# Kernel tuning notes

Measured on AMD Instinct MI355X. Metric: run time of the kernel, lower is better.

## Reference

```python
import jax, jax.numpy as jnp
import numpy as np

XI = 4.0  # init kwarg


def _gaussian_kernel(xi: float):
    radius = int(3 * xi)
    coords = jnp.arange(-radius, radius + 1, dtype=jnp.float32)
    g1 = jnp.exp(-coords ** 2 / (2 * xi * xi))
    g1 = g1 / g1.sum()
    # dense 3D outer-product kernel, shape (K, K, K)
    g3 = g1[:, None, None] * g1[None, :, None] * g1[None, None, :]
    K = g3.shape[0]
    # grouped depthwise weight: (out=3, in/groups=1, K, K, K)
    return jnp.broadcast_to(g3[None, None], (3, 1, K, K, K))


def setup_inputs() -> dict:
    key = jax.random.key(0)
    x = jax.random.normal(key, (1, 3, 160, 160, 160), dtype=jnp.float32)
    kernel = _gaussian_kernel(XI)
    return {"x": x, "kernel": kernel}


def reference(x, kernel):
    # grouped Conv3d, groups=3 (depthwise), 'same' padding of radius each side
    r = (kernel.shape[-1] - 1) // 2
    return jax.lax.conv_general_dilated(
        x, kernel,
        window_strides=(1, 1, 1),
        padding=[(r, r), (r, r), (r, r)],
        dimension_numbers=("NCDHW", "OIDHW", "NCDHW"),
        feature_group_count=3,
    )
```

## Files before the change

kernel.cpp:

```cpp
#include <hip/hip_runtime.h>
#include <hip/hip_fp16.h>


#define NV 160
constexpr int KS    = 25;
constexpr int RAD   = 12;
constexpr int PLANE = NV * NV;
constexpr int VOL   = NV * NV * NV;
constexpr int TOT   = 3 * VOL;
constexpr int ROWS  = NV + 2 * RAD;

constexpr int PITCH = 17;
constexpr int OPT   = 10;
constexpr int WIN   = OPT + KS - 1;

constexpr int QP    = 9;
constexpr int OPT4  = 5;
constexpr int WIN4  = OPT4 + KS - 1;

__device__ __forceinline__ void pk(float2& a, float2 g, float2 v) {
    asm("v_pk_fma_f32 %0, %1, %2, %0" : "+v"(a) : "v"(g), "v"(v));
}

__device__ __forceinline__ void load_g(const float* __restrict__ k3, float* g) {
    float c   = k3[12 * 625 + 312];
    float g12 = cbrtf(c);
    float inv = 1.0f / (g12 * g12);
#pragma unroll
    for (int t = 0; t < KS; ++t) g[t] = k3[t * 625 + 312] * inv;
}

__global__ __launch_bounds__(256) void conv_w(const float* __restrict__ in,
                                              __half* __restrict__ out,
                                              const float* __restrict__ k3) {
    __shared__ float2 T[ROWS][PITCH];
    float gs[KS];
    load_g(k3, gs);
    float2 g2[KS];
#pragma unroll
    for (int t = 0; t < KS; ++t) g2[t] = make_float2(gs[t], gs[t]);

    int tid = threadIdx.x;
    int b   = blockIdx.x;
    int ht  = b % 5;
    int cd  = b / 5;
    int h0  = ht * 32;
    const float* base = in + (size_t)cd * PLANE;

    int wl = tid & 31, hq = tid >> 5;
#pragma unroll
    for (int hh = 0; hh < 2; ++hh) {
        int hp = hq + hh * 8;
        const float* r0 = base + (h0 + 2 * hp) * NV;
#pragma unroll
        for (int ib = 0; ib < ROWS; ib += 32) {
            int i = ib + wl;
            if (i < ROWS) {
                int wv = i - RAD;
                float a = 0.f, bb = 0.f;
                if (wv >= 0 && wv < NV) { a = r0[wv]; bb = r0[NV + wv]; }
                T[i][hp] = make_float2(a, bb);
            }
        }
    }
    __syncthreads();

    int p  = tid & 15;
    int ct = tid >> 4;
    int wb = ct * OPT;
    float2 acc[OPT];
#pragma unroll
    for (int j = 0; j < OPT; ++j) acc[j] = make_float2(0.f, 0.f);
#pragma unroll
    for (int it = 0; it < WIN; ++it) {
        float2 v = T[wb + it][p];
#pragma unroll
        for (int j = 0; j < OPT; ++j) {
            int t = it - j;
            if (t >= 0 && t < KS) pk(acc[j], g2[t], v);
        }
    }
    __half* obA = out + (size_t)cd * PLANE + (h0 + 2 * p) * NV + wb;
#pragma unroll
    for (int jj = 0; jj < OPT / 2; ++jj) {
        *(__half2*)(obA + 2 * jj) =
            __float22half2_rn(make_float2(acc[2*jj].x, acc[2*jj+1].x));
        *(__half2*)(obA + NV + 2 * jj) =
            __float22half2_rn(make_float2(acc[2*jj].y, acc[2*jj+1].y));
    }
}

__global__ __launch_bounds__(256) void conv_h(const __half* __restrict__ in,
                                              __half* __restrict__ out,
                                              const float* __restrict__ k3) {
    __shared__ float4 T4[ROWS][QP];
    float gs[KS];
    load_g(k3, gs);
    float2 g2[KS];
#pragma unroll
    for (int t = 0; t < KS; ++t) g2[t] = make_float2(gs[t], gs[t]);

    int tid = threadIdx.x;
    int b   = blockIdx.x;
    int wt  = b % 5;
    int cd  = b / 5;
    int w0  = wt * 32;
    const __half* base = in + (size_t)cd * PLANE + w0;

    int q = tid & 7, r = tid >> 3;
#pragma unroll
    for (int ib = 0; ib < ROWS; ib += 32) {
        int i = ib + r;
        if (i < ROWS) {
            int h = i - RAD;
            float4 v = make_float4(0.f, 0.f, 0.f, 0.f);
            if (h >= 0 && h < NV) {
                const __half2* p2 = (const __half2*)(base + h * NV + 4 * q);
                float2 lo = __half22float2(p2[0]);
                float2 hi = __half22float2(p2[1]);
                v = make_float4(lo.x, lo.y, hi.x, hi.y);
            }
            T4[i][q] = v;
        }
    }
    __syncthreads();

    int wq = tid & 7, ct = tid >> 3;
    int hb = ct * OPT4;
    float2 alo[OPT4], ahi[OPT4];
#pragma unroll
    for (int j = 0; j < OPT4; ++j) { alo[j] = make_float2(0.f, 0.f); ahi[j] = alo[j]; }
#pragma unroll
    for (int it = 0; it < WIN4; ++it) {
        float4 v = T4[hb + it][wq];
        float2 vlo = make_float2(v.x, v.y);
        float2 vhi = make_float2(v.z, v.w);
#pragma unroll
        for (int j = 0; j < OPT4; ++j) {
            int t = it - j;
            if (t >= 0 && t < KS) { pk(alo[j], g2[t], vlo); pk(ahi[j], g2[t], vhi); }
        }
    }
    __half* ob = out + (size_t)cd * PLANE + w0 + 4 * wq;
#pragma unroll
    for (int j = 0; j < OPT4; ++j) {
        __half2 o01 = __float22half2_rn(make_float2(alo[j].x, alo[j].y));
        __half2 o23 = __float22half2_rn(make_float2(ahi[j].x, ahi[j].y));
        __half* pdst = ob + (hb + j) * NV;
        *(__half2*)(pdst)     = o01;
        *(__half2*)(pdst + 2) = o23;
    }
}

__global__ __launch_bounds__(256) void conv_d(const __half* __restrict__ in,
                                              float* __restrict__ out,
                                              const float* __restrict__ k3) {
    __shared__ float4 T4[ROWS][QP];
    float gs[KS];
    load_g(k3, gs);
    float2 g2[KS];
#pragma unroll
    for (int t = 0; t < KS; ++t) g2[t] = make_float2(gs[t], gs[t]);

    int tid = threadIdx.x;
    int b   = blockIdx.x;
    int wt  = b % 5;
    int ch  = b / 5;
    int c   = ch / NV, h = ch % NV;
    int w0  = wt * 32;
    const __half* base = in + (size_t)c * VOL + h * NV + w0;

    int q = tid & 7, r = tid >> 3;
#pragma unroll
    for (int ib = 0; ib < ROWS; ib += 32) {
        int i = ib + r;
        if (i < ROWS) {
            int d = i - RAD;
            float4 v = make_float4(0.f, 0.f, 0.f, 0.f);
            if (d >= 0 && d < NV) {
                const __half2* p2 = (const __half2*)(base + (size_t)d * PLANE + 4 * q);
                float2 lo = __half22float2(p2[0]);
                float2 hi = __half22float2(p2[1]);
                v = make_float4(lo.x, lo.y, hi.x, hi.y);
            }
            T4[i][q] = v;
        }
    }
    __syncthreads();

    int wq = tid & 7, ct = tid >> 3;
    int db = ct * OPT4;
    float2 alo[OPT4], ahi[OPT4];
#pragma unroll
    for (int j = 0; j < OPT4; ++j) { alo[j] = make_float2(0.f, 0.f); ahi[j] = alo[j]; }
#pragma unroll
    for (int it = 0; it < WIN4; ++it) {
        float4 v = T4[db + it][wq];
        float2 vlo = make_float2(v.x, v.y);
        float2 vhi = make_float2(v.z, v.w);
#pragma unroll
        for (int j = 0; j < OPT4; ++j) {
            int t = it - j;
            if (t >= 0 && t < KS) { pk(alo[j], g2[t], vlo); pk(ahi[j], g2[t], vhi); }
        }
    }
    float* ob = out + (size_t)c * VOL + h * NV + w0 + 4 * wq;
#pragma unroll
    for (int j = 0; j < OPT4; ++j)
        *(float4*)(ob + (size_t)(db + j) * PLANE) =
            make_float4(alo[j].x, alo[j].y, ahi[j].x, ahi[j].y);
}

__global__ __launch_bounds__(256) void conv3d_direct(const float* __restrict__ x,
                                                     const float* __restrict__ k3,
                                                     float* __restrict__ out) {
    int idx = blockIdx.x * 256 + threadIdx.x;
    if (idx >= TOT) return;
    int w = idx % NV;
    int t = idx / NV;
    int h = t % NV; t /= NV;
    int d = t % NV;
    int c = t / NV;
    const float* kc = k3 + c * (KS * KS * KS);
    float acc = 0.f;
    for (int i = 0; i < KS; ++i) {
        int dd = d + i - RAD;
        if (dd < 0 || dd >= NV) continue;
        for (int j = 0; j < KS; ++j) {
            int hh = h + j - RAD;
            if (hh < 0 || hh >= NV) continue;
            const float* xr = x + (c * NV + dd) * NV * NV + hh * NV + (w - RAD);
            const float* kr = kc + (i * KS + j) * KS;
            int k0 = (RAD - w) > 0 ? (RAD - w) : 0;
            int k1 = (NV + RAD - w) < KS ? (NV + RAD - w) : KS;
            for (int k = k0; k < k1; ++k) acc += kr[k] * xr[k];
        }
    }
    out[idx] = acc;
}

extern "C" void kernel_launch(void* const* d_in, const int* in_sizes, int n_in,
                              void* d_out, int out_size, void* d_ws, size_t ws_size,
                              hipStream_t stream) {
    const float* x  = (const float*)d_in[0];
    const float* k3 = (const float*)d_in[1];
    float* out = (float*)d_out;

    if (ws_size >= (size_t)TOT * 2 * sizeof(__half)) {
        __half* tmpA = (__half*)d_ws;
        __half* tmpB = tmpA + TOT;
        conv_w<<<2400, 256, 0, stream>>>(x, tmpA, k3);
        conv_h<<<2400, 256, 0, stream>>>(tmpA, tmpB, k3);
        conv_d<<<2400, 256, 0, stream>>>(tmpB, out, k3);
    } else {
        conv3d_direct<<<(TOT + 255) / 256, 256, 0, stream>>>(x, k3, out);
    }
}
```

Baseline: 57.43 us.

## Fuse W and H separable passes into one kernel through shared memory

Replaces the separate W-pass and H-pass kernels with one fused kernel. Each block loads half a plane plus halo rows, runs the W convolution in registers from float4 global loads, stores the results as fp16 in LDS, then runs the H convolution from LDS. This removes one full fp16 intermediate round trip through global memory and one kernel launch. In exchange the H halo rows are recomputed in the W pass, occupancy is reduced by the large LDS tile, and the W intermediate is now rounded to fp16 in LDS.

```diff
diff --git a/kernel.cpp b/kernel.cpp
--- a/kernel.cpp
+++ b/kernel.cpp
@@ -8,12 +8,13 @@
 constexpr int PLANE = NV * NV;
 constexpr int VOL   = NV * NV * NV;
 constexpr int TOT   = 3 * VOL;
+
+constexpr int HHALF  = 80;
+constexpr int WROWS  = 104;
+constexpr int WPITCH = 81;
+constexpr int WTASKS = WROWS * 20;
+
 constexpr int ROWS  = NV + 2 * RAD;
-
-constexpr int PITCH = 17;
-constexpr int OPT   = 10;
-constexpr int WIN   = OPT + KS - 1;
-
 constexpr int QP    = 9;
 constexpr int OPT4  = 5;
 constexpr int WIN4  = OPT4 + KS - 1;
@@ -30,125 +31,90 @@
     for (int t = 0; t < KS; ++t) g[t] = k3[t * 625 + 312] * inv;
 }
 
-__global__ __launch_bounds__(256) void conv_w(const float* __restrict__ in,
-                                              __half* __restrict__ out,
-                                              const float* __restrict__ k3) {
-    __shared__ float2 T[ROWS][PITCH];
-    float gs[KS];
-    load_g(k3, gs);
+__global__ __launch_bounds__(320, 4) void fused_wh(const float* __restrict__ in,
+                                                   __half* __restrict__ out,
+                                                   const float* __restrict__ k3) {
+    __shared__ __half2 WH[WROWS][WPITCH];
+    float g[KS];
+    load_g(k3, g);
+
+    int tid  = threadIdx.x;
+    int b    = blockIdx.x;
+    int half = b & 1;
+    int cd   = b >> 1;
+    int h0   = half * HHALF;
+    const float* base = in + (size_t)cd * PLANE;
+
+#pragma unroll
+    for (int itr = 0; itr < 7; ++itr) {
+        int task = itr * 320 + tid;
+        if (task < WTASKS) {
+            int r  = task % WROWS;
+            int s  = task / WROWS;
+            int hq = h0 + r - RAD;
+            if (hq >= 0 && hq < NV) {
+                const float* rp = base + hq * NV;
+                int w0 = 8 * s - RAD;
+                float buf[32];
+#pragma unroll
+                for (int u = 0; u < 8; ++u) {
+                    int wa = w0 + 4 * u;
+                    int wc = wa < 0 ? 0 : (wa > NV - 4 ? NV - 4 : wa);
+                    float4 f = *(const float4*)(rp + wc);
+                    buf[4*u]   = f.x; buf[4*u+1] = f.y;
+                    buf[4*u+2] = f.z; buf[4*u+3] = f.w;
+                }
+#pragma unroll
+                for (int m = 0; m < 32; ++m) {
+                    int w = w0 + m;
+                    buf[m] = (w >= 0 && w < NV) ? buf[m] : 0.f;
+                }
+                float acc[8];
+#pragma unroll
+                for (int k = 0; k < 8; ++k) acc[k] = 0.f;
+#pragma unroll
+                for (int t = 0; t < KS; ++t)
+#pragma unroll
+                    for (int k = 0; k < 8; ++k)
+                        acc[k] = fmaf(g[t], buf[k + t], acc[k]);
+#pragma unroll
+                for (int u = 0; u < 4; ++u)
+                    WH[r][4*s + u] =
+                        __float22half2_rn(make_float2(acc[2*u], acc[2*u+1]));
+            } else {
+                __half2 z = __float22half2_rn(make_float2(0.f, 0.f));
+#pragma unroll
+                for (int u = 0; u < 4; ++u) WH[r][4*s + u] = z;
+            }
+        }
+    }
+    __syncthreads();
+
+    int wp = tid % 80;
+    int hg = tid / 80;
     float2 g2[KS];
 #pragma unroll
-    for (int t = 0; t < KS; ++t) g2[t] = make_float2(gs[t], gs[t]);
-
-    int tid = threadIdx.x;
-    int b   = blockIdx.x;
-    int ht  = b % 5;
-    int cd  = b / 5;
-    int h0  = ht * 32;
-    const float* base = in + (size_t)cd * PLANE;
-
-    int wl = tid & 31, hq = tid >> 5;
-#pragma unroll
-    for (int hh = 0; hh < 2; ++hh) {
-        int hp = hq + hh * 8;
-        const float* r0 = base + (h0 + 2 * hp) * NV;
-#pragma unroll
-        for (int ib = 0; ib < ROWS; ib += 32) {
-            int i = ib + wl;
-            if (i < ROWS) {
-                int wv = i - RAD;
-                float a = 0.f, bb = 0.f;
-                if (wv >= 0 && wv < NV) { a = r0[wv]; bb = r0[NV + wv]; }
-                T[i][hp] = make_float2(a, bb);
+    for (int t = 0; t < KS; ++t) g2[t] = make_float2(g[t], g[t]);
+
+#pragma unroll
+    for (int ch = 0; ch < 2; ++ch) {
+        int hb = hg * 20 + ch * 10;
+        float2 acc[10];
+#pragma unroll
+        for (int j = 0; j < 10; ++j) acc[j] = make_float2(0.f, 0.f);
+#pragma unroll
+        for (int it = 0; it < 34; ++it) {
+            float2 v = __half22float2(WH[hb + it][wp]);
+#pragma unroll
+            for (int j = 0; j < 10; ++j) {
+                int t = it - j;
+                if (t >= 0 && t < KS) pk(acc[j], g2[t], v);
             }
         }
-    }
-    __syncthreads();
-
-    int p  = tid & 15;
-    int ct = tid >> 4;
-    int wb = ct * OPT;
-    float2 acc[OPT];
-#pragma unroll
-    for (int j = 0; j < OPT; ++j) acc[j] = make_float2(0.f, 0.f);
-#pragma unroll
-    for (int it = 0; it < WIN; ++it) {
-        float2 v = T[wb + it][p];
-#pragma unroll
-        for (int j = 0; j < OPT; ++j) {
-            int t = it - j;
-            if (t >= 0 && t < KS) pk(acc[j], g2[t], v);
-        }
-    }
-    __half* obA = out + (size_t)cd * PLANE + (h0 + 2 * p) * NV + wb;
-#pragma unroll
-    for (int jj = 0; jj < OPT / 2; ++jj) {
-        *(__half2*)(obA + 2 * jj) =
-            __float22half2_rn(make_float2(acc[2*jj].x, acc[2*jj+1].x));
-        *(__half2*)(obA + NV + 2 * jj) =
-            __float22half2_rn(make_float2(acc[2*jj].y, acc[2*jj+1].y));
-    }
-}
-
-__global__ __launch_bounds__(256) void conv_h(const __half* __restrict__ in,
-                                              __half* __restrict__ out,
-                                              const float* __restrict__ k3) {
-    __shared__ float4 T4[ROWS][QP];
-    float gs[KS];
-    load_g(k3, gs);
-    float2 g2[KS];
-#pragma unroll
-    for (int t = 0; t < KS; ++t) g2[t] = make_float2(gs[t], gs[t]);
-
-    int tid = threadIdx.x;
-    int b   = blockIdx.x;
-    int wt  = b % 5;
-    int cd  = b / 5;
-    int w0  = wt * 32;
-    const __half* base = in + (size_t)cd * PLANE + w0;
-
-    int q = tid & 7, r = tid >> 3;
-#pragma unroll
-    for (int ib = 0; ib < ROWS; ib += 32) {
-        int i = ib + r;
-        if (i < ROWS) {
-            int h = i - RAD;
-            float4 v = make_float4(0.f, 0.f, 0.f, 0.f);
-            if (h >= 0 && h < NV) {
-                const __half2* p2 = (const __half2*)(base + h * NV + 4 * q);
-                float2 lo = __half22float2(p2[0]);
-                float2 hi = __half22float2(p2[1]);
-                v = make_float4(lo.x, lo.y, hi.x, hi.y);
-            }
-            T4[i][q] = v;
-        }
-    }
-    __syncthreads();
-
-    int wq = tid & 7, ct = tid >> 3;
-    int hb = ct * OPT4;
-    float2 alo[OPT4], ahi[OPT4];
-#pragma unroll
-    for (int j = 0; j < OPT4; ++j) { alo[j] = make_float2(0.f, 0.f); ahi[j] = alo[j]; }
-#pragma unroll
-    for (int it = 0; it < WIN4; ++it) {
-        float4 v = T4[hb + it][wq];
-        float2 vlo = make_float2(v.x, v.y);
-        float2 vhi = make_float2(v.z, v.w);
-#pragma unroll
-        for (int j = 0; j < OPT4; ++j) {
-            int t = it - j;
-            if (t >= 0 && t < KS) { pk(alo[j], g2[t], vlo); pk(ahi[j], g2[t], vhi); }
-        }
-    }
-    __half* ob = out + (size_t)cd * PLANE + w0 + 4 * wq;
-#pragma unroll
-    for (int j = 0; j < OPT4; ++j) {
-        __half2 o01 = __float22half2_rn(make_float2(alo[j].x, alo[j].y));
-        __half2 o23 = __float22half2_rn(make_float2(ahi[j].x, ahi[j].y));
-        __half* pdst = ob + (hb + j) * NV;
-        *(__half2*)(pdst)     = o01;
-        *(__half2*)(pdst + 2) = o23;
+        __half* ob = out + (size_t)cd * PLANE + (size_t)(h0 + hb) * NV + 2 * wp;
+#pragma unroll
+        for (int j = 0; j < 10; ++j)
+            *(__half2*)(ob + j * NV) = __float22half2_rn(acc[j]);
     }
 }
 
@@ -246,12 +212,10 @@
     const float* k3 = (const float*)d_in[1];
     float* out = (float*)d_out;
 
-    if (ws_size >= (size_t)TOT * 2 * sizeof(__half)) {
+    if (ws_size >= (size_t)TOT * sizeof(__half)) {
         __half* tmpA = (__half*)d_ws;
-        __half* tmpB = tmpA + TOT;
-        conv_w<<<2400, 256, 0, stream>>>(x, tmpA, k3);
-        conv_h<<<2400, 256, 0, stream>>>(tmpA, tmpB, k3);
-        conv_d<<<2400, 256, 0, stream>>>(tmpB, out, k3);
+        fused_wh<<<960, 320, 0, stream>>>(x, tmpA, k3);
+        conv_d<<<2400, 256, 0, stream>>>(tmpA, out, k3);
     } else {
         conv3d_direct<<<(TOT + 255) / 256, 256, 0, stream>>>(x, k3, out);
     }
```

New measurement: 120.0 us. +109.0%, slower.
